# Performance work log

Measured on AMD Instinct MI355X. Metric: run time of the kernel, lower is better.

Reference implementation:

```python
import jax, jax.numpy as jnp
import numpy as np

D_MODEL = 1024
NUM_HEADS = 16
D_K = D_MODEL // NUM_HEADS


def setup_inputs() -> dict:
    key = jax.random.key(0)
    ks = jax.random.split(key, 11)
    B, S = 2, 2048
    scale = 1.0 / np.sqrt(D_MODEL)
    inp = {
        "q": jax.random.normal(ks[0], (B, S, D_MODEL), jnp.float32),
        "k": jax.random.normal(ks[1], (B, S, D_MODEL), jnp.float32),
        "v": jax.random.normal(ks[2], (B, S, D_MODEL), jnp.float32),
        "wq": jax.random.normal(ks[3], (D_MODEL, D_MODEL), jnp.float32) * scale,
        "bq": jax.random.normal(ks[4], (D_MODEL,), jnp.float32) * 0.01,
        "wk": jax.random.normal(ks[5], (D_MODEL, D_MODEL), jnp.float32) * scale,
        "bk": jax.random.normal(ks[6], (D_MODEL,), jnp.float32) * 0.01,
        "wv": jax.random.normal(ks[7], (D_MODEL, D_MODEL), jnp.float32) * scale,
        "bv": jax.random.normal(ks[8], (D_MODEL,), jnp.float32) * 0.01,
        "wo": jax.random.normal(ks[9], (D_MODEL, D_MODEL), jnp.float32) * scale,
        "bo": jax.random.normal(ks[10], (D_MODEL,), jnp.float32) * 0.01,
    }
    return inp


def reference(q, k, v, wq, bq, wk, bk, wv, bv, wo, bo):
    B, S, _ = q.shape
    # Linear projections (torch Linear: x @ W.T + b). Weights stored [out, in].
    qh = (q @ wq.T + bq).reshape(B, S, NUM_HEADS, D_K).transpose(0, 2, 1, 3)  # [B,H,S,dk]
    kh = (k @ wk.T + bk).reshape(B, S, NUM_HEADS, D_K).transpose(0, 2, 1, 3)
    vh = (v @ wv.T + bv).reshape(B, S, NUM_HEADS, D_K).transpose(0, 2, 1, 3)
    scores = jnp.einsum("bhqd,bhkd->bhqk", qh, kh) / jnp.sqrt(jnp.asarray(D_K, qh.dtype))
    weights = jax.nn.softmax(scores, axis=-1)
    attn = jnp.einsum("bhqk,bhkd->bhqd", weights, vh)  # [B,H,S,dk]
    attn = attn.transpose(0, 2, 1, 3).reshape(B, S, D_MODEL)
    return attn @ wo.T + bo
```

## Files before the change

### kernel.cpp

```cpp
#include <hip/hip_runtime.h>

#define DM 1024
#define NH 16
#define DK 64
#define BB 2
#define SS 2048
#define MT (BB*SS)

typedef __attribute__((ext_vector_type(8))) short bf16x8;
typedef __attribute__((ext_vector_type(4))) float f32x4;

#define QSCALE 0.1803368801111191f
#define EXPC  (-14.426950408889634f)

__device__ __forceinline__ unsigned short f2bf(float f) {
    unsigned int u = __float_as_uint(f);
    u += 0x7FFF + ((u >> 16) & 1);
    return (unsigned short)(u >> 16);
}

__device__ __forceinline__ unsigned int cvt_pk_bf16(float lo, float hi) {
    unsigned int r;
    asm("v_cvt_pk_bf16_f32 %0, %1, %2" : "=v"(r) : "v"(lo), "v"(hi));
    return r;
}

__device__ __forceinline__ void mfma16(f32x4& acc, uint2 a, uint2 b) {
    asm("v_mfma_f32_16x16x16_bf16 %0, %1, %2, %0" : "+v"(acc) : "v"(a), "v"(b));
}

__device__ __forceinline__ void gload16(const void* g, void* l) {
    __builtin_amdgcn_global_load_lds(
        (const __attribute__((address_space(1))) unsigned int*)g,
        (__attribute__((address_space(3))) unsigned int*)(unsigned int)(unsigned long long)l,
        16, 0, 0);
}

struct CvtArgs {
    const float* s[7];
    unsigned short* d[7];
    int n[7];
    float scl[7];
};

__global__ __launch_bounds__(256) void cvt_f32_bf16(CvtArgs a) {
    const int arr = blockIdx.y;
    const int i = (blockIdx.x * 256 + threadIdx.x) * 8;
    if (i >= a.n[arr]) return;
    const float sc = a.scl[arr];
    const float4* sp = (const float4*)(a.s[arr] + i);
    float4 x = sp[0], y = sp[1];
    union { unsigned short us[8]; uint4 u4; } r;
    r.us[0] = f2bf(x.x * sc); r.us[1] = f2bf(x.y * sc);
    r.us[2] = f2bf(x.z * sc); r.us[3] = f2bf(x.w * sc);
    r.us[4] = f2bf(y.x * sc); r.us[5] = f2bf(y.y * sc);
    r.us[6] = f2bf(y.z * sc); r.us[7] = f2bf(y.w * sc);
    *(uint4*)(a.d[arr] + i) = r.u4;
}

struct ProjArgs {
    const unsigned short* A[3];
    const unsigned short* B[3];
    const float* bias[3];
    unsigned short* out[3];
    float bscale[3];
};

__global__ __launch_bounds__(256, 3) void proj3(ProjArgs pa) {
    __shared__ __align__(16) unsigned short As[2][128 * 32];
    __shared__ __align__(16) unsigned short Bs[2][128 * 32];

    const int z = blockIdx.y;
    const int bx = blockIdx.x;
    const int m0 = (z < 2 ? (bx >> 3) : (bx >> 5)) * 128;
    const int n0 = (z < 2 ? (bx & 7) : (bx & 31)) * 128;
    const unsigned short* A = pa.A[z];
    const unsigned short* B = pa.B[z];
    const float* bias = pa.bias[z];
    const float bsc = pa.bscale[z];
    unsigned short* out = pa.out[z];

    const int tid = (int)threadIdx.x;
    const int l = tid & 63;
    const int w = tid >> 6;
    const int wm = w >> 1, wn = w & 1;

    const int strow = l >> 2;
    const int sslot = (l & 3) ^ ((l >> 3) & 3);
    const int fr = l & 15, fj = l >> 4;
    const int swz = ((fj ^ ((fr >> 1) & 3)) << 4);

    const f32x4 zero = {0.f, 0.f, 0.f, 0.f};
    f32x4 acc[4][4];
    #pragma unroll
    for (int mf = 0; mf < 4; ++mf)
        #pragma unroll
        for (int nf = 0; nf < 4; ++nf) acc[mf][nf] = zero;

    #pragma unroll
    for (int t = 0; t < 2; ++t) {
        const int c = w * 2 + t;
        const int row = c * 16 + strow;
        gload16(A + (size_t)(m0 + row) * DM + sslot * 8, (char*)As[0] + c * 1024);
        gload16(B + (size_t)(n0 + row) * DM + sslot * 8, (char*)Bs[0] + c * 1024);
    }
    __syncthreads();

    for (int kt = 0; kt < DM; kt += 32) {
        const int cb = (kt >> 5) & 1;
        if (kt + 32 < DM) {
            #pragma unroll
            for (int t = 0; t < 2; ++t) {
                const int c = w * 2 + t;
                const int row = c * 16 + strow;
                gload16(A + (size_t)(m0 + row) * DM + (kt + 32) + sslot * 8, (char*)As[cb ^ 1] + c * 1024);
                gload16(B + (size_t)(n0 + row) * DM + (kt + 32) + sslot * 8, (char*)Bs[cb ^ 1] + c * 1024);
            }
        }
        bf16x8 af[4], bfr[4];
        #pragma unroll
        for (int mf = 0; mf < 4; ++mf)
            af[mf] = *(const bf16x8*)((const char*)As[cb] + (wm * 64 + mf * 16 + fr) * 64 + swz);
        #pragma unroll
        for (int nf = 0; nf < 4; ++nf)
            bfr[nf] = *(const bf16x8*)((const char*)Bs[cb] + (wn * 64 + nf * 16 + fr) * 64 + swz);
        #pragma unroll
        for (int mf = 0; mf < 4; ++mf)
            #pragma unroll
            for (int nf = 0; nf < 4; ++nf)
                acc[mf][nf] = __builtin_amdgcn_mfma_f32_16x16x32_bf16(af[mf], bfr[nf], acc[mf][nf], 0, 0, 0);
        __syncthreads();
    }

    #pragma unroll
    for (int nf = 0; nf < 4; ++nf) {
        const int n = n0 + wn * 64 + nf * 16 + fr;
        const float bn = (z == 2) ? 0.f : bias[n] * bsc;
        #pragma unroll
        for (int mf = 0; mf < 4; ++mf) {
            #pragma unroll
            for (int j = 0; j < 4; ++j) {
                const int m = m0 + wm * 64 + mf * 16 + fj * 4 + j;
                if (z < 2) {
                    const float val = acc[mf][nf][j] + bn;
                    out[((size_t)((m >> 11) * NH + (n >> 6)) * SS + (m & (SS - 1))) * DK + (n & 63)] = f2bf(val);
                } else {
                    const float val = acc[mf][nf][j] + bias[m];
                    out[(size_t)((n >> 11) * NH + (m >> 6)) * (SS * DK) + (size_t)(m & 63) * SS + (n & (SS - 1))] = f2bf(val);
                }
            }
        }
    }
}

__global__ __launch_bounds__(256, 2) void gemm_out(
    const unsigned short* __restrict__ A,
    const unsigned short* __restrict__ B,
    const float* __restrict__ bias,
    float* __restrict__ out)
{
    __shared__ __align__(16) unsigned short As[2][128 * 32];
    __shared__ __align__(16) unsigned short Bs[2][64 * 32];

    const int tid = (int)threadIdx.x;
    const int l = tid & 63;
    const int w = tid >> 6;
    const int wm = w >> 1, wn = w & 1;
    const int m0 = blockIdx.x * 128, n0 = blockIdx.y * 64;

    const int strow = l >> 2;
    const int sslot = (l & 3) ^ ((l >> 3) & 3);
    const int fr = l & 15, fj = l >> 4;
    const int swz = ((fj ^ ((fr >> 1) & 3)) << 4);

    const f32x4 zero = {0.f, 0.f, 0.f, 0.f};
    f32x4 acc[4][2];
    #pragma unroll
    for (int mf = 0; mf < 4; ++mf)
        #pragma unroll
        for (int nf = 0; nf < 2; ++nf) acc[mf][nf] = zero;

    #pragma unroll
    for (int t = 0; t < 2; ++t) {
        const int c = w * 2 + t;
        gload16(A + (size_t)(m0 + c * 16 + strow) * DM + sslot * 8, (char*)As[0] + c * 1024);
    }
    gload16(B + (size_t)(n0 + w * 16 + strow) * DM + sslot * 8, (char*)Bs[0] + w * 1024);
    __syncthreads();

    for (int kt = 0; kt < DM; kt += 32) {
        const int cb = (kt >> 5) & 1;
        if (kt + 32 < DM) {
            #pragma unroll
            for (int t = 0; t < 2; ++t) {
                const int c = w * 2 + t;
                gload16(A + (size_t)(m0 + c * 16 + strow) * DM + (kt + 32) + sslot * 8, (char*)As[cb ^ 1] + c * 1024);
            }
            gload16(B + (size_t)(n0 + w * 16 + strow) * DM + (kt + 32) + sslot * 8, (char*)Bs[cb ^ 1] + w * 1024);
        }
        bf16x8 af[4], bfr[2];
        #pragma unroll
        for (int mf = 0; mf < 4; ++mf)
            af[mf] = *(const bf16x8*)((const char*)As[cb] + (wm * 64 + mf * 16 + fr) * 64 + swz);
        #pragma unroll
        for (int nf = 0; nf < 2; ++nf)
            bfr[nf] = *(const bf16x8*)((const char*)Bs[cb] + (wn * 32 + nf * 16 + fr) * 64 + swz);
        #pragma unroll
        for (int mf = 0; mf < 4; ++mf)
            #pragma unroll
            for (int nf = 0; nf < 2; ++nf)
                acc[mf][nf] = __builtin_amdgcn_mfma_f32_16x16x32_bf16(af[mf], bfr[nf], acc[mf][nf], 0, 0, 0);
        __syncthreads();
    }

    #pragma unroll
    for (int nf = 0; nf < 2; ++nf) {
        const int n = n0 + wn * 32 + nf * 16 + fr;
        const float bn = bias[n];
        #pragma unroll
        for (int mf = 0; mf < 4; ++mf)
            #pragma unroll
            for (int j = 0; j < 4; ++j) {
                const int m = m0 + wm * 64 + mf * 16 + fj * 4 + j;
                out[(size_t)m * DM + n] = acc[mf][nf][j] + bn;
            }
    }
}

__global__ __launch_bounds__(256, 2) void attn_bf16(
    const unsigned short* __restrict__ qh,
    const unsigned short* __restrict__ kh,
    const unsigned short* __restrict__ vt,
    unsigned short* __restrict__ ao)
{
    __shared__ __align__(16) unsigned short Ks[2][64 * 64];
    __shared__ __align__(16) unsigned short Vs[2][64 * 64];

    const int tid = (int)threadIdx.x;
    const int l = tid & 63;
    const int w = tid >> 6;
    const int bh = blockIdx.x;
    const int q0 = blockIdx.y * 128;
    const size_t pb = (size_t)bh * (SS * DK);

    const int fr = l & 15, fj = l >> 4;
    const int s8 = fr & 7;
    const int strow = l >> 3;
    const int sslot = (l & 7) ^ strow;

    bf16x8 qreg[2][2];
    #pragma unroll
    for (int qf = 0; qf < 2; ++qf)
        #pragma unroll
        for (int ks = 0; ks < 2; ++ks)
            qreg[qf][ks] = *(const bf16x8*)(qh + pb + (size_t)(q0 + w * 32 + qf * 16 + fr) * DK + ks * 32 + fj * 8);

    #pragma unroll
    for (int t = 0; t < 2; ++t) {
        const int c = w * 2 + t;
        gload16(kh + pb + (size_t)(c * 8 + strow) * DK + sslot * 8, (char*)Ks[0] + c * 1024);
        gload16(vt + pb + (size_t)(c * 8 + strow) * SS + sslot * 8, (char*)Vs[0] + c * 1024);
    }
    asm volatile("s_waitcnt vmcnt(0)" ::: "memory");
    __syncthreads();

    const f32x4 zero = {0.f, 0.f, 0.f, 0.f};
    f32x4 ot[4][2];
    f32x4 lacc[2];
    #pragma unroll
    for (int nf = 0; nf < 4; ++nf)
        #pragma unroll
        for (int qf = 0; qf < 2; ++qf) ot[nf][qf] = zero;
    lacc[0] = zero; lacc[1] = zero;

    const int NT = SS / 64;
    for (int t = 0; t < NT; ++t) {
        const int c = t & 1;
        if (t + 1 < NT) {
            #pragma unroll
            for (int tt = 0; tt < 2; ++tt) {
                const int ch = w * 2 + tt;
                gload16(kh + pb + (size_t)((t + 1) * 64 + ch * 8 + strow) * DK + sslot * 8,
                        (char*)Ks[c ^ 1] + ch * 1024);
            }
        }
        f32x4 sc[4][2];
        #pragma unroll
        for (int kf = 0; kf < 4; ++kf)
            #pragma unroll
            for (int qf = 0; qf < 2; ++qf) sc[kf][qf] = zero;
        __builtin_amdgcn_s_setprio(1);
        #pragma unroll
        for (int ks = 0; ks < 2; ++ks) {
            bf16x8 kfr[4];
            #pragma unroll
            for (int kf = 0; kf < 4; ++kf)
                kfr[kf] = *(const bf16x8*)((const char*)Ks[c] + (kf * 16 + fr) * 128 + (((ks * 4 + fj) ^ s8) << 4));
            #pragma unroll
            for (int kf = 0; kf < 4; ++kf)
                #pragma unroll
                for (int qf = 0; qf < 2; ++qf)
                    sc[kf][qf] = __builtin_amdgcn_mfma_f32_16x16x32_bf16(kfr[kf], qreg[qf][ks], sc[kf][qf], 0, 0, 0);
        }
        __builtin_amdgcn_s_setprio(0);

        uint2 pp[4][2];
        #pragma unroll
        for (int qf = 0; qf < 2; ++qf) {
            #pragma unroll
            for (int kf = 0; kf < 4; ++kf) {
                const float e0 = __builtin_amdgcn_exp2f(sc[kf][qf][0] + EXPC);
                const float e1 = __builtin_amdgcn_exp2f(sc[kf][qf][1] + EXPC);
                const float e2 = __builtin_amdgcn_exp2f(sc[kf][qf][2] + EXPC);
                const float e3 = __builtin_amdgcn_exp2f(sc[kf][qf][3] + EXPC);
                lacc[qf][0] += e0; lacc[qf][1] += e1;
                lacc[qf][2] += e2; lacc[qf][3] += e3;
                pp[kf][qf].x = cvt_pk_bf16(e0, e1);
                pp[kf][qf].y = cvt_pk_bf16(e2, e3);
            }
        }

        __builtin_amdgcn_sched_barrier(0);
        asm volatile("s_waitcnt vmcnt(0) lgkmcnt(0)" ::: "memory");
        __builtin_amdgcn_s_barrier();
        __builtin_amdgcn_sched_barrier(0);

        if (t + 1 < NT) {
            #pragma unroll
            for (int tt = 0; tt < 2; ++tt) {
                const int ch = w * 2 + tt;
                gload16(vt + pb + (size_t)(ch * 8 + strow) * SS + (t + 1) * 64 + sslot * 8,
                        (char*)Vs[c ^ 1] + ch * 1024);
            }
        }

        __builtin_amdgcn_s_setprio(1);
        #pragma unroll
        for (int kf = 0; kf < 4; ++kf) {
            #pragma unroll
            for (int nf = 0; nf < 4; ++nf) {
                const uint2 vf = *(const uint2*)((const char*)Vs[c] + (nf * 16 + fr) * 128
                                   + (((2 * kf + (fj >> 1)) ^ s8) << 4) + ((fj & 1) << 3));
                #pragma unroll
                for (int qf = 0; qf < 2; ++qf)
                    mfma16(ot[nf][qf], vf, pp[kf][qf]);
            }
        }
        __builtin_amdgcn_s_setprio(0);
    }

    float inv[2];
    #pragma unroll
    for (int qf = 0; qf < 2; ++qf) {
        float s = (lacc[qf][0] + lacc[qf][1]) + (lacc[qf][2] + lacc[qf][3]);
        s += __shfl_xor(s, 16);
        s += __shfl_xor(s, 32);
        inv[qf] = 1.0f / s;
    }
    const int b = bh >> 4, h = bh & 15;
    #pragma unroll
    for (int qf = 0; qf < 2; ++qf) {
        const int qg = q0 + w * 32 + qf * 16 + fr;
        unsigned short* dst = ao + (size_t)(b * SS + qg) * DM + h * DK + fj * 4;
        #pragma unroll
        for (int nf = 0; nf < 4; ++nf) {
            uint2 pw;
            pw.x = cvt_pk_bf16(ot[nf][qf][0] * inv[qf], ot[nf][qf][1] * inv[qf]);
            pw.y = cvt_pk_bf16(ot[nf][qf][2] * inv[qf], ot[nf][qf][3] * inv[qf]);
            *(uint2*)(dst + nf * 16) = pw;
        }
    }
}

extern "C" void kernel_launch(void* const* d_in, const int* in_sizes, int n_in,
                              void* d_out, int out_size, void* d_ws, size_t ws_size,
                              hipStream_t stream) {
    const float* q  = (const float*)d_in[0];
    const float* k  = (const float*)d_in[1];
    const float* v  = (const float*)d_in[2];
    const float* wq = (const float*)d_in[3];
    const float* bq = (const float*)d_in[4];
    const float* wk = (const float*)d_in[5];
    const float* bk = (const float*)d_in[6];
    const float* wv = (const float*)d_in[7];
    const float* bv = (const float*)d_in[8];
    const float* wo = (const float*)d_in[9];
    const float* bo = (const float*)d_in[10];

    const size_t NQ = (size_t)MT * DM;
    const size_t NW = (size_t)DM * DM;
    unsigned short* wsb = (unsigned short*)d_ws;
    unsigned short* qb  = wsb;
    unsigned short* kb  = qb  + NQ;
    unsigned short* vb  = kb  + NQ;
    unsigned short* wqb = vb  + NQ;
    unsigned short* wkb = wqb + NW;
    unsigned short* wvb = wkb + NW;
    unsigned short* wob = wvb + NW;
    unsigned short* qhb = wob + NW;
    unsigned short* khb = qhb + NQ;
    unsigned short* vtb = khb + NQ;
    unsigned short* aob = vtb + NQ;

    CvtArgs ca;
    ca.s[0] = q;  ca.d[0] = qb;  ca.n[0] = (int)NQ; ca.scl[0] = 1.f;
    ca.s[1] = k;  ca.d[1] = kb;  ca.n[1] = (int)NQ; ca.scl[1] = 1.f;
    ca.s[2] = v;  ca.d[2] = vb;  ca.n[2] = (int)NQ; ca.scl[2] = 1.f;
    ca.s[3] = wq; ca.d[3] = wqb; ca.n[3] = (int)NW; ca.scl[3] = QSCALE;
    ca.s[4] = wk; ca.d[4] = wkb; ca.n[4] = (int)NW; ca.scl[4] = 1.f;
    ca.s[5] = wv; ca.d[5] = wvb; ca.n[5] = (int)NW; ca.scl[5] = 1.f;
    ca.s[6] = wo; ca.d[6] = wob; ca.n[6] = (int)NW; ca.scl[6] = 1.f;
    cvt_f32_bf16<<<dim3(2048, 7), dim3(256), 0, stream>>>(ca);

    ProjArgs pa;
    pa.A[0] = qb;  pa.B[0] = wqb; pa.bias[0] = bq; pa.out[0] = qhb; pa.bscale[0] = QSCALE;
    pa.A[1] = kb;  pa.B[1] = wkb; pa.bias[1] = bk; pa.out[1] = khb; pa.bscale[1] = 1.f;
    pa.A[2] = wvb; pa.B[2] = vb;  pa.bias[2] = bv; pa.out[2] = vtb; pa.bscale[2] = 1.f;
    proj3<<<dim3(256, 3), dim3(256), 0, stream>>>(pa);

    attn_bf16<<<dim3(32, 16), dim3(256), 0, stream>>>(qhb, khb, vtb, aob);

    gemm_out<<<dim3(32, 16), dim3(256), 0, stream>>>(aob, wob, bo, (float*)d_out);
}
```

Before: 126.2 us.

## Use 16x16x32 bf16 MFMA for PV product via permuted K row order

The K projection now writes rows in a permuted sequence order, so the score fragments from QK^T line up with the 16x16x32 MFMA operand layout. The P·V product therefore uses half as many 16x16x32 MFMAs instead of 16x16x16 ones, with 16-byte V loads from LDS. This aims to raise matrix-core throughput and cut LDS read instructions in the attention inner loop. It depends on the permutation matching across the projection and attention kernels. A mismatch would corrupt the output.

```diff
diff --git a/kernel.cpp b/kernel.cpp
--- a/kernel.cpp
+++ b/kernel.cpp
@@ -25,15 +25,15 @@
     return r;
 }
 
-__device__ __forceinline__ void mfma16(f32x4& acc, uint2 a, uint2 b) {
-    asm("v_mfma_f32_16x16x16_bf16 %0, %1, %2, %0" : "+v"(acc) : "v"(a), "v"(b));
-}
-
 __device__ __forceinline__ void gload16(const void* g, void* l) {
     __builtin_amdgcn_global_load_lds(
         (const __attribute__((address_space(1))) unsigned int*)g,
         (__attribute__((address_space(3))) unsigned int*)(unsigned int)(unsigned long long)l,
         16, 0, 0);
+}
+
+__device__ __forceinline__ int kperm(int s) {
+    return (s & ~31) | (((s >> 2) & 1) << 4) | (((s >> 3) & 3) << 2) | (s & 3);
 }
 
 struct CvtArgs {
@@ -143,7 +143,9 @@
                 const int m = m0 + wm * 64 + mf * 16 + fj * 4 + j;
                 if (z < 2) {
                     const float val = acc[mf][nf][j] + bn;
-                    out[((size_t)((m >> 11) * NH + (n >> 6)) * SS + (m & (SS - 1))) * DK + (n & 63)] = f2bf(val);
+                    int s = m & (SS - 1);
+                    if (z == 1) s = kperm(s);
+                    out[((size_t)((m >> 11) * NH + (n >> 6)) * SS + s) * DK + (n & 63)] = f2bf(val);
                 } else {
                     const float val = acc[mf][nf][j] + bias[m];
                     out[(size_t)((n >> 11) * NH + (m >> 6)) * (SS * DK) + (size_t)(m & 63) * SS + (n & (SS - 1))] = f2bf(val);
@@ -304,19 +306,25 @@
         }
         __builtin_amdgcn_s_setprio(0);
 
-        uint2 pp[4][2];
+        bf16x8 pbf[2][2];
         #pragma unroll
         for (int qf = 0; qf < 2; ++qf) {
             #pragma unroll
-            for (int kf = 0; kf < 4; ++kf) {
-                const float e0 = __builtin_amdgcn_exp2f(sc[kf][qf][0] + EXPC);
-                const float e1 = __builtin_amdgcn_exp2f(sc[kf][qf][1] + EXPC);
-                const float e2 = __builtin_amdgcn_exp2f(sc[kf][qf][2] + EXPC);
-                const float e3 = __builtin_amdgcn_exp2f(sc[kf][qf][3] + EXPC);
-                lacc[qf][0] += e0; lacc[qf][1] += e1;
-                lacc[qf][2] += e2; lacc[qf][3] += e3;
-                pp[kf][qf].x = cvt_pk_bf16(e0, e1);
-                pp[kf][qf].y = cvt_pk_bf16(e2, e3);
+            for (int ks = 0; ks < 2; ++ks) {
+                union { unsigned int u[4]; bf16x8 v; } pk;
+                #pragma unroll
+                for (int kf = 0; kf < 2; ++kf) {
+                    const f32x4 s4 = sc[ks * 2 + kf][qf];
+                    const float e0 = __builtin_amdgcn_exp2f(s4[0] + EXPC);
+                    const float e1 = __builtin_amdgcn_exp2f(s4[1] + EXPC);
+                    const float e2 = __builtin_amdgcn_exp2f(s4[2] + EXPC);
+                    const float e3 = __builtin_amdgcn_exp2f(s4[3] + EXPC);
+                    lacc[qf][0] += e0; lacc[qf][1] += e1;
+                    lacc[qf][2] += e2; lacc[qf][3] += e3;
+                    pk.u[kf * 2 + 0] = cvt_pk_bf16(e0, e1);
+                    pk.u[kf * 2 + 1] = cvt_pk_bf16(e2, e3);
+                }
+                pbf[qf][ks] = pk.v;
             }
         }
 
@@ -336,15 +344,16 @@
 
         __builtin_amdgcn_s_setprio(1);
         #pragma unroll
-        for (int kf = 0; kf < 4; ++kf) {
-            #pragma unroll
-            for (int nf = 0; nf < 4; ++nf) {
-                const uint2 vf = *(const uint2*)((const char*)Vs[c] + (nf * 16 + fr) * 128
-                                   + (((2 * kf + (fj >> 1)) ^ s8) << 4) + ((fj & 1) << 3));
+        for (int ks = 0; ks < 2; ++ks) {
+            bf16x8 va[4];
+            #pragma unroll
+            for (int nf = 0; nf < 4; ++nf)
+                va[nf] = *(const bf16x8*)((const char*)Vs[c] + (nf * 16 + fr) * 128 + (((ks * 4 + fj) ^ s8) << 4));
+            #pragma unroll
+            for (int nf = 0; nf < 4; ++nf)
                 #pragma unroll
                 for (int qf = 0; qf < 2; ++qf)
-                    mfma16(ot[nf][qf], vf, pp[kf][qf]);
-            }
+                    ot[nf][qf] = __builtin_amdgcn_mfma_f32_16x16x32_bf16(va[nf], pbf[qf][ks], ot[nf][qf], 0, 0, 0);
         }
         __builtin_amdgcn_s_setprio(0);
     }
```

Measured after the change: 119.0 us. -5.7%, faster.
